# Kernel tuning notes

Hardware: AMD Instinct MI355X
Metric: run time of the kernel (lower is better)

## Reference

```python
import jax, jax.numpy as jnp
import numpy as np

L = 6        # num_coupling_layers
T_DIM = 64   # t_dim
HALF = T_DIM // 2
COND = 128   # cond_dim
HID = 1024   # hidden_dim
B = 32768


def setup_inputs() -> dict:
    key = jax.random.key(0)
    ks = jax.random.split(key, 8)
    s_in = 1.0 / np.sqrt(HALF + COND)
    s_h = 1.0 / np.sqrt(HID)
    T = jax.random.normal(ks[0], (B, T_DIM), dtype=jnp.float32)
    cond = jax.random.normal(ks[1], (B, COND), dtype=jnp.float32)
    W1 = jax.random.normal(ks[2], (L, HALF + COND, HID), dtype=jnp.float32) * s_in
    b1 = jnp.zeros((L, HID), dtype=jnp.float32)
    W2 = jax.random.normal(ks[3], (L, HID, HID), dtype=jnp.float32) * s_h
    b2 = jnp.zeros((L, HID), dtype=jnp.float32)
    W3 = jax.random.normal(ks[4], (L, HID, 2 * HALF), dtype=jnp.float32) * s_h
    b3 = jnp.zeros((L, 2 * HALF), dtype=jnp.float32)
    return {"T": T, "cond": cond, "W1": W1, "b1": b1, "W2": W2, "b2": b2, "W3": W3, "b3": b3}


def reference(T, cond, W1, b1, W2, b2, W3, b3):
    # Conditional normalizing flow: 6 affine coupling layers with alternating
    # contiguous half masks. Even layers transform the first half, odd the second.
    def mlp(h, i):
        x = jax.nn.relu(h @ W1[i] + b1[i])
        x = jax.nn.relu(x @ W2[i] + b2[i])
        return x @ W3[i] + b3[i]

    z = T
    log_det = jnp.zeros(T.shape[0], dtype=T.dtype)
    for i in range(L):
        if i % 2 == 0:
            masked, unmasked = z[:, :HALF], z[:, HALF:]
        else:
            masked, unmasked = z[:, HALF:], z[:, :HALF]
        params = mlp(jnp.concatenate([unmasked, cond], axis=1), i)
        s = jnp.tanh(params[:, :HALF])
        t_shift = params[:, HALF:]
        y_masked = masked * jnp.exp(s) + t_shift
        if i % 2 == 0:
            z = jnp.concatenate([y_masked, unmasked], axis=1)
        else:
            z = jnp.concatenate([unmasked, y_masked], axis=1)
        log_det = log_det + jnp.sum(s, axis=1)
    return z, log_det
```

## Files before the change

### kernel.cpp

```cpp
#include <hip/hip_runtime.h>
#include <hip/hip_fp16.h>
#include <stdint.h>

typedef _Float16 f16;
typedef _Float16 f16x8 __attribute__((ext_vector_type(8)));
typedef float f32x4 __attribute__((ext_vector_type(4)));

#define NB 32768
#define LAYERS 6
#define AK 160
#define HID 1024

__device__ __forceinline__ void async_copy16(const void* g, void* l) {
  __builtin_amdgcn_global_load_lds(
      (const __attribute__((address_space(1))) void*)g,
      (__attribute__((address_space(3))) void*)l, 16, 0, 0);
}

__device__ __forceinline__ void wtrans_tile(const float* __restrict__ W,
                                            f16* __restrict__ Wt,
                                            const int K_, const int N_,
                                            const int bx, const int by,
                                            const int bz, float (*t)[65])
{
  const long off = (long)bz * K_ * N_;
  const float* Wl = W + off;
  f16* Wtl = Wt + off;
  const int k0 = by * 64, n0 = bx * 64;
  const int tx = threadIdx.x & 63, ty4 = threadIdx.x >> 6;
#pragma unroll
  for (int r = ty4; r < 64; r += 4) {
    const int k = k0 + r;
    if (k < K_) t[r][tx] = Wl[(long)k * N_ + n0 + tx];
  }
  __syncthreads();
  const int k = k0 + tx;
  if (k < K_) {
#pragma unroll
    for (int r = ty4; r < 64; r += 4) {
      const int n = n0 + r;
      Wtl[(long)n * K_ + k] = (f16)t[tx][r];
    }
  }
}

__global__ void prep_all(const float* __restrict__ T, const float* __restrict__ cond,
                         const float* __restrict__ W1, const float* __restrict__ W2,
                         const float* __restrict__ W3,
                         float* __restrict__ z, float* __restrict__ ld,
                         f16* __restrict__ A,
                         f16* __restrict__ W1t, f16* __restrict__ W2t,
                         f16* __restrict__ W3t)
{
  __shared__ float t[64][65];
  const int b = blockIdx.x;
  if (b < 2048) {
    const int S1 = NB * 64;
    const int S2 = S1 + NB;
    const int S3 = S2 + NB * 32;
    const int S4 = S3 + NB * 128;
    for (int i = b * blockDim.x + threadIdx.x; i < S4; i += 2048 * blockDim.x) {
      if (i < S1) {
        z[i] = T[i];
      } else if (i < S2) {
        ld[i - S1] = 0.0f;
      } else if (i < S3) {
        int r = i - S2;
        int row = r >> 5, j = r & 31;
        A[(size_t)row * AK + j] = (f16)T[row * 64 + 32 + j];
      } else {
        int r = i - S3;
        int row = r >> 7, j = r & 127;
        A[(size_t)row * AK + 32 + j] = (f16)cond[r];
      }
    }
  } else if (b < 2048 + 288) {
    const int l = b - 2048;
    wtrans_tile(W1, W1t, AK, 1024, l % 16, (l / 16) % 3, l / 48, t);
  } else if (b < 2048 + 288 + 1536) {
    const int l = b - (2048 + 288);
    wtrans_tile(W2, W2t, HID, 1024, l % 16, (l / 16) % 16, l / 256, t);
  } else {
    const int l = b - (2048 + 288 + 1536);
    wtrans_tile(W3, W3t, HID, 64, 0, l % 16, l / 16, t);
  }
}

__global__ __launch_bounds__(256, 2)
void gemm1_full(const f16* __restrict__ A,
                const f16* __restrict__ Wt,
                const float* __restrict__ bias,
                f16* __restrict__ C)
{
  __shared__ __align__(16) f16 As[128 * 160];
  __shared__ __align__(16) f16 Bs[128 * 160];
  const int tid  = threadIdx.x;
  const int lane = tid & 63;
  const int wave = tid >> 6;
  const int c15  = lane & 15;
  const int quad = lane >> 4;
  const int wm = (wave & 1) * 64;
  const int wn = (wave >> 1) * 64;

  const int b = blockIdx.x;
  const int x = b & 7, i = b >> 3;
  const long rowStart = (long)(x * 32 + (i >> 3)) * 128;
  const long colStart = (long)(i & 7) * 128;

  const f16* Ab = A  + rowStart * AK;
  const f16* Bb = Wt + colStart * AK;

#pragma unroll
  for (int it = 0; it < 10; ++it) {
    const int f = it * 256 + tid;
    const int row = f / 20;
    const int ch  = f - row * 20;
    const int chs = ch ^ ((row >> 1) & 3);
    async_copy16(Ab + (long)row * AK + chs * 8, &As[0] + (long)f * 8);
    async_copy16(Bb + (long)row * AK + chs * 8, &Bs[0] + (long)f * 8);
  }
  __syncthreads();

  f32x4 acc[4][4] = {};
#pragma unroll
  for (int kt = 0; kt < 5; ++kt) {
    f16x8 a[4], bf[4];
#pragma unroll
    for (int mi = 0; mi < 4; ++mi) {
      const int R = wm + mi * 16 + c15;
      a[mi] = *(const f16x8*)&As[(R * 20 + kt * 4 + (quad ^ ((R >> 1) & 3))) * 8];
    }
#pragma unroll
    for (int ni = 0; ni < 4; ++ni) {
      const int R = wn + ni * 16 + c15;
      bf[ni] = *(const f16x8*)&Bs[(R * 20 + kt * 4 + (quad ^ ((R >> 1) & 3))) * 8];
    }
#pragma unroll
    for (int mi = 0; mi < 4; ++mi)
#pragma unroll
      for (int ni = 0; ni < 4; ++ni)
        acc[mi][ni] = __builtin_amdgcn_mfma_f32_16x16x32_f16(
            a[mi], bf[ni], acc[mi][ni], 0, 0, 0);
  }

#pragma unroll
  for (int ni = 0; ni < 4; ++ni) {
    const long gn = colStart + wn + ni * 16 + c15;
    const float bv = bias[gn];
#pragma unroll
    for (int mi = 0; mi < 4; ++mi) {
#pragma unroll
      for (int r = 0; r < 4; ++r) {
        const long gm = rowStart + wm + mi * 16 + quad * 4 + r;
        float v = acc[mi][ni][r] + bv;
        v = fmaxf(v, 0.0f);
        C[gm * HID + gn] = (f16)v;
      }
    }
  }
}

__global__ __launch_bounds__(512, 2)
void gemm2_sp(const f16* __restrict__ A,
              const f16* __restrict__ Wt,
              const float* __restrict__ bias,
              f16* __restrict__ C)
{
  __shared__ __align__(16) f16 As[2][8192];
  __shared__ __align__(16) f16 Bs[2][8192];

  const int tid  = threadIdx.x;
  const int lane = tid & 63;
  const int wave = tid >> 6;
  const int c15  = lane & 15;
  const int quad = lane >> 4;
  const int wm = (wave >> 2) * 128;
  const int wn = (wave & 3) * 64;

  const int b = blockIdx.x;
  const int wgid = (b & 7) * 64 + (b >> 3);
  const long rowStart = (long)(wgid >> 2) * 256;
  const long colStart = (long)(wgid & 3) * 256;

  const f16* Ab = A  + rowStart * HID;
  const f16* Bb = Wt + colStart * HID;

  const int r0  = tid >> 2;
  const int ch0 = tid & 3;
  const long g0 = (long)r0 * HID + (((ch0 ^ ((r0 >> 1) & 3))) << 3);
  const int l0 = tid << 3;

  auto stageFull = [&](int kt2, int sel) {
    const f16* sa = Ab + (long)kt2 * 32;
    const f16* sb = Bb + (long)kt2 * 32;
    f16* da = &As[sel][0];
    f16* db = &Bs[sel][0];
    async_copy16(sa + g0,                  da + l0);
    async_copy16(sa + (long)128 * HID + g0, da + 4096 + l0);
    async_copy16(sb + g0,                  db + l0);
    async_copy16(sb + (long)128 * HID + g0, db + 4096 + l0);
  };

  stageFull(0, 0);
  stageFull(1, 1);
  asm volatile("s_waitcnt vmcnt(4)" ::: "memory");
  __builtin_amdgcn_s_barrier();
  __builtin_amdgcn_sched_barrier(0);

  f32x4 acc[8][4] = {};

#pragma unroll 2
  for (int kt = 0; kt < 32; ++kt) {
    const int sel = kt & 1;
    const f16* as = &As[sel][0];
    const f16* bs = &Bs[sel][0];
    const int ktp2 = (kt + 2 < 32) ? kt + 2 : 31;

    f16x8 a[8], bf[4];
#pragma unroll
    for (int m = 0; m < 8; ++m) {
      const int r = wm + m * 16 + c15;
      a[m] = *(const f16x8*)&as[r * 32 + ((quad ^ ((r >> 1) & 3)) << 3)];
    }
#pragma unroll
    for (int n = 0; n < 4; ++n) {
      const int r = wn + n * 16 + c15;
      bf[n] = *(const f16x8*)&bs[r * 32 + ((quad ^ ((r >> 1) & 3)) << 3)];
    }
    asm volatile("s_waitcnt lgkmcnt(0)" ::: "memory");
    __builtin_amdgcn_s_barrier();
    stageFull(ktp2, sel);
    __builtin_amdgcn_sched_barrier(0);
    __builtin_amdgcn_s_setprio(1);
#pragma unroll
    for (int m = 0; m < 8; ++m)
#pragma unroll
      for (int n = 0; n < 4; ++n)
        acc[m][n] = __builtin_amdgcn_mfma_f32_16x16x32_f16(
            a[m], bf[n], acc[m][n], 0, 0, 0);
    __builtin_amdgcn_s_setprio(0);
    __builtin_amdgcn_sched_barrier(0);
    asm volatile("s_waitcnt vmcnt(4)" ::: "memory");
    __builtin_amdgcn_s_barrier();
  }

#pragma unroll
  for (int n = 0; n < 4; ++n) {
    const long gn = colStart + wn + n * 16 + c15;
    const float bv = bias[gn];
#pragma unroll
    for (int m = 0; m < 8; ++m) {
#pragma unroll
      for (int r = 0; r < 4; ++r) {
        const long gm = rowStart + wm + m * 16 + quad * 4 + r;
        float v = acc[m][n][r] + bv;
        C[gm * HID + gn] = (f16)fmaxf(v, 0.0f);
      }
    }
  }
}

__global__ __launch_bounds__(256, 2)
void gemm3_coupling(const f16* __restrict__ X2, const f16* __restrict__ W3t,
                    const float* __restrict__ b3, float* __restrict__ z,
                    float* __restrict__ log_det, f16* __restrict__ Anext,
                    const int maskoff)
{
  __shared__ __align__(16) f16 As[2][64 * 64];
  __shared__ __align__(16) f16 Bs[2][64 * 64];
  const int tid = threadIdx.x;
  const int wave = tid >> 6, lane = tid & 63;
  const int c15 = lane & 15, quad = lane >> 4;
  const int wm = wave * 16;
  const long rowStart = (long)blockIdx.x * 64;

  const f16* Ab = X2 + rowStart * HID;
  const int brow = tid >> 3;
  const int bkc  = ((tid & 7) ^ (brow & 7)) * 8;

  f32x4 acc[4] = {};

  auto stage = [&](int c, int sel) {
    const long kb = (long)c * 64;
#pragma unroll
    for (int q = 0; q < 2; ++q) {
      async_copy16(Ab  + (long)(q * 32 + brow) * HID + kb + bkc,
                   &As[sel][0] + (q * 256 + wave * 64) * 8);
      async_copy16(W3t + (long)(q * 32 + brow) * HID + kb + bkc,
                   &Bs[sel][0] + (q * 256 + wave * 64) * 8);
    }
  };

  stage(0, 0);
  for (int c = 0; c < 16; ++c) {
    __syncthreads();
    if (c + 1 < 16) stage(c + 1, (c + 1) & 1);
    const f16* as = &As[c & 1][0];
    const f16* bs = &Bs[c & 1][0];

#pragma unroll
    for (int s = 0; s < 2; ++s) {
      const int Ra = wm + c15;
      f16x8 a = *(const f16x8*)&as[(Ra * 8 + ((s * 4 + quad) ^ (Ra & 7))) * 8];
      f16x8 bf[4];
#pragma unroll
      for (int ni = 0; ni < 4; ++ni) {
        const int R = ni * 16 + c15;
        bf[ni] = *(const f16x8*)&bs[(R * 8 + ((s * 4 + quad) ^ (R & 7))) * 8];
      }
#pragma unroll
      for (int ni = 0; ni < 4; ++ni)
        acc[ni] = __builtin_amdgcn_mfma_f32_16x16x32_f16(a, bf[ni], acc[ni], 0, 0, 0);
    }
  }

  float sp[4] = {0.0f, 0.0f, 0.0f, 0.0f};
#pragma unroll
  for (int ni = 0; ni < 2; ++ni) {
    const int j = ni * 16 + c15;
    const float bs = b3[j];
    const float bt = b3[32 + j];
#pragma unroll
    for (int r = 0; r < 4; ++r) {
      const long gm = rowStart + wm + quad * 4 + r;
      const float sv = acc[ni][r] + bs;
      const float e2 = __expf(2.0f * sv);
      const float s  = 1.0f - 2.0f / (e2 + 1.0f);
      const float tv = acc[ni + 2][r] + bt;
      const float m  = z[gm * 64 + maskoff + j];
      const float y  = fmaf(m, __expf(s), tv);
      z[gm * 64 + maskoff + j] = y;
      Anext[gm * AK + j] = (f16)y;
      sp[r] += s;
    }
  }
#pragma unroll
  for (int r = 0; r < 4; ++r) {
    float v = sp[r];
    v += __shfl_xor(v, 1);
    v += __shfl_xor(v, 2);
    v += __shfl_xor(v, 4);
    v += __shfl_xor(v, 8);
    if (c15 == 0) {
      const long gm = rowStart + wm + quad * 4 + r;
      log_det[gm] += v;
    }
  }
}

extern "C" void kernel_launch(void* const* d_in, const int* in_sizes, int n_in,
                              void* d_out, int out_size, void* d_ws, size_t ws_size,
                              hipStream_t stream) {
  (void)in_sizes; (void)n_in; (void)out_size; (void)ws_size;
  const float* T    = (const float*)d_in[0];
  const float* cond = (const float*)d_in[1];
  const float* W1   = (const float*)d_in[2];
  const float* b1   = (const float*)d_in[3];
  const float* W2   = (const float*)d_in[4];
  const float* b2   = (const float*)d_in[5];
  const float* W3   = (const float*)d_in[6];
  const float* b3   = (const float*)d_in[7];

  float* z  = (float*)d_out;
  float* ld = z + (size_t)NB * 64;

  f16* A   = (f16*)d_ws;
  f16* X1  = A   + (size_t)NB * AK;
  f16* X2  = X1  + (size_t)NB * HID;
  f16* W1t = X2  + (size_t)NB * HID;
  f16* W2t = W1t + (size_t)6 * 1024 * 160;
  f16* W3t = W2t + ((size_t)6 << 20);

  prep_all<<<3968, 256, 0, stream>>>(T, cond, W1, W2, W3,
                                     z, ld, A, W1t, W2t, W3t);

  const int g1 = (NB / 128) * (HID / 128);
  const int g2 = (NB / 256) * (HID / 256);
  for (int l = 0; l < LAYERS; ++l) {
    gemm1_full<<<g1, 256, 0, stream>>>(A, W1t + (size_t)l * 1024 * AK,
                                       b1 + l * 1024, X1);
    gemm2_sp<<<g2, 512, 0, stream>>>(X1, W2t + ((size_t)l << 20),
                                     b2 + l * 1024, X2);
    const int maskoff = (l & 1) ? 32 : 0;
    gemm3_coupling<<<NB / 64, 256, 0, stream>>>(X2, W3t + (size_t)l * 64 * 1024,
                                                b3 + l * 64, z, ld, A, maskoff);
  }
}
```

Measured before the change: 811.5 us.

## Restructure hidden GEMM into 8-phase ping-pong pipeline with K=64 tiles

```diff
diff --git a/kernel.cpp b/kernel.cpp
--- a/kernel.cpp
+++ b/kernel.cpp
@@ -160,14 +160,44 @@
   }
 }
 
+#define RD_A(dst, base, mq) \
+  _Pragma("unroll") \
+  for (int mi = 0; mi < 4; ++mi) { \
+    const int r_ = wm + (mq) * 64 + mi * 16 + c15; \
+    _Pragma("unroll") \
+    for (int ks = 0; ks < 2; ++ks) \
+      dst[mi][ks] = *(const f16x8*)&(base)[r_ * 64 + ((((ks << 2) + quad) ^ (r_ & 7)) << 3)]; \
+  }
+#define RD_B(dst, base, nq) \
+  _Pragma("unroll") \
+  for (int ni = 0; ni < 2; ++ni) { \
+    const int r_ = wn + (nq) * 32 + ni * 16 + c15; \
+    _Pragma("unroll") \
+    for (int ks = 0; ks < 2; ++ks) \
+      dst[ni][ks] = *(const f16x8*)&(base)[r_ * 64 + ((((ks << 2) + quad) ^ (r_ & 7)) << 3)]; \
+  }
+#define MM(am, an, afr, bfr) \
+  __builtin_amdgcn_s_setprio(1); \
+  _Pragma("unroll") \
+  for (int ks = 0; ks < 2; ++ks) \
+  _Pragma("unroll") \
+  for (int mi = 0; mi < 4; ++mi) \
+  _Pragma("unroll") \
+  for (int ni = 0; ni < 2; ++ni) \
+    acc[(am) + mi][(an) + ni] = __builtin_amdgcn_mfma_f32_16x16x32_f16( \
+        afr[mi][ks], bfr[ni][ks], acc[(am) + mi][(an) + ni], 0, 0, 0); \
+  __builtin_amdgcn_s_setprio(0);
+#define BARRIER __builtin_amdgcn_s_barrier()
+#define LGKM0   asm volatile("s_waitcnt lgkmcnt(0)")
+
 __global__ __launch_bounds__(512, 2)
-void gemm2_sp(const f16* __restrict__ A,
+void gemm2_8p(const f16* __restrict__ A,
               const f16* __restrict__ Wt,
               const float* __restrict__ bias,
               f16* __restrict__ C)
 {
-  __shared__ __align__(16) f16 As[2][8192];
-  __shared__ __align__(16) f16 Bs[2][8192];
+  __shared__ __align__(16) f16 As[2][16384];
+  __shared__ __align__(16) f16 Bs[2][16384];
 
   const int tid  = threadIdx.x;
   const int lane = tid & 63;
@@ -185,75 +215,106 @@
   const f16* Ab = A  + rowStart * HID;
   const f16* Bb = Wt + colStart * HID;
 
-  const int r0  = tid >> 2;
-  const int ch0 = tid & 3;
-  const long g0 = (long)r0 * HID + (((ch0 ^ ((r0 >> 1) & 3))) << 3);
+  const int rh0 = tid >> 3;
+  const int ch0 = tid & 7;
+  const long g0 = (long)rh0 * HID + ((ch0 ^ (rh0 & 7)) << 3);
+  const long g1 = (long)(64 + rh0) * HID + ((ch0 ^ ((64 + rh0) & 7)) << 3);
   const int l0 = tid << 3;
-
-  auto stageFull = [&](int kt2, int sel) {
-    const f16* sa = Ab + (long)kt2 * 32;
-    const f16* sb = Bb + (long)kt2 * 32;
-    f16* da = &As[sel][0];
-    f16* db = &Bs[sel][0];
-    async_copy16(sa + g0,                  da + l0);
-    async_copy16(sa + (long)128 * HID + g0, da + 4096 + l0);
-    async_copy16(sb + g0,                  db + l0);
-    async_copy16(sb + (long)128 * HID + g0, db + 4096 + l0);
+  const int l1 = (512 + tid) << 3;
+
+  auto stA = [&](int kt, int h) {
+    const f16* src = Ab + (long)h * 128 * HID + (long)kt * 64;
+    f16* dst = &As[kt & 1][h * 8192];
+    async_copy16(src + g0, dst + l0);
+    async_copy16(src + g1, dst + l1);
   };
-
-  stageFull(0, 0);
-  stageFull(1, 1);
-  asm volatile("s_waitcnt vmcnt(4)" ::: "memory");
-  __builtin_amdgcn_s_barrier();
-  __builtin_amdgcn_sched_barrier(0);
+  auto stB = [&](int kt, int h) {
+    const f16* src = Bb + (long)h * 128 * HID + (long)kt * 64;
+    f16* dst = &Bs[kt & 1][h * 8192];
+    async_copy16(src + g0, dst + l0);
+    async_copy16(src + g1, dst + l1);
+  };
+
+  stB(0, 0); stA(0, 0); stB(0, 1); stA(0, 1);
+  stB(1, 0); stA(1, 0);
+  asm volatile("s_waitcnt vmcnt(4)");
+  BARRIER;
 
   f32x4 acc[8][4] = {};
 
-#pragma unroll 2
-  for (int kt = 0; kt < 32; ++kt) {
-    const int sel = kt & 1;
-    const f16* as = &As[sel][0];
-    const f16* bs = &Bs[sel][0];
-    const int ktp2 = (kt + 2 < 32) ? kt + 2 : 31;
-
-    f16x8 a[8], bf[4];
-#pragma unroll
-    for (int m = 0; m < 8; ++m) {
-      const int r = wm + m * 16 + c15;
-      a[m] = *(const f16x8*)&as[r * 32 + ((quad ^ ((r >> 1) & 3)) << 3)];
-    }
-#pragma unroll
-    for (int n = 0; n < 4; ++n) {
-      const int r = wn + n * 16 + c15;
-      bf[n] = *(const f16x8*)&bs[r * 32 + ((quad ^ ((r >> 1) & 3)) << 3)];
-    }
-    asm volatile("s_waitcnt lgkmcnt(0)" ::: "memory");
-    __builtin_amdgcn_s_barrier();
-    stageFull(ktp2, sel);
-    __builtin_amdgcn_sched_barrier(0);
-    __builtin_amdgcn_s_setprio(1);
-#pragma unroll
-    for (int m = 0; m < 8; ++m)
-#pragma unroll
-      for (int n = 0; n < 4; ++n)
-        acc[m][n] = __builtin_amdgcn_mfma_f32_16x16x32_f16(
-            a[m], bf[n], acc[m][n], 0, 0, 0);
-    __builtin_amdgcn_s_setprio(0);
-    __builtin_amdgcn_sched_barrier(0);
-    asm volatile("s_waitcnt vmcnt(4)" ::: "memory");
-    __builtin_amdgcn_s_barrier();
-  }
-
-#pragma unroll
-  for (int n = 0; n < 4; ++n) {
-    const long gn = colStart + wn + n * 16 + c15;
+#pragma unroll 1
+  for (int t = 0; t < 8; ++t) {
+    const int kt0 = 2 * t, kt1 = 2 * t + 1;
+    const f16* asx = &As[0][0];
+    const f16* bsx = &Bs[0][0];
+    const f16* asy = &As[1][0];
+    const f16* bsy = &Bs[1][0];
+    const bool pre = (t < 7);
+    f16x8 a0[4][2], a1[4][2], b0[2][2], b1[2][2];
+
+    RD_A(a0, asx, 0);
+    RD_B(b0, bsx, 0);
+    stB(kt1, 1);
+    BARRIER; LGKM0;
+    MM(0, 0, a0, b0);
+    BARRIER;
+
+    RD_B(b1, bsx, 1);
+    stA(kt1, 1);
+    BARRIER; LGKM0;
+    MM(0, 2, a0, b1);
+    BARRIER;
+
+    RD_A(a1, asx, 1);
+    if (pre) stB(kt0 + 2, 0);
+    BARRIER; LGKM0;
+    MM(4, 0, a1, b0);
+    BARRIER;
+
+    if (pre) stA(kt0 + 2, 0);
+    MM(4, 2, a1, b1);
+    if (pre) { asm volatile("s_waitcnt vmcnt(4)"); }
+    else     { asm volatile("s_waitcnt vmcnt(0)"); }
+    BARRIER;
+
+    RD_A(a0, asy, 0);
+    RD_B(b0, bsy, 0);
+    if (pre) stB(kt0 + 2, 1);
+    BARRIER; LGKM0;
+    MM(0, 0, a0, b0);
+    BARRIER;
+
+    RD_B(b1, bsy, 1);
+    if (pre) stA(kt0 + 2, 1);
+    BARRIER; LGKM0;
+    MM(0, 2, a0, b1);
+    BARRIER;
+
+    RD_A(a1, asy, 1);
+    if (pre) stB(kt1 + 2, 0);
+    BARRIER; LGKM0;
+    MM(4, 0, a1, b0);
+    BARRIER;
+
+    if (pre) stA(kt1 + 2, 0);
+    MM(4, 2, a1, b1);
+    if (pre) { asm volatile("s_waitcnt vmcnt(4)"); }
+    else     { asm volatile("s_waitcnt vmcnt(0)"); }
+    BARRIER;
+  }
+
+#pragma unroll
+  for (int nii = 0; nii < 4; ++nii) {
+    const int nof = (nii >> 1) * 32 + (nii & 1) * 16;
+    const long gn = colStart + wn + nof + c15;
     const float bv = bias[gn];
 #pragma unroll
-    for (int m = 0; m < 8; ++m) {
+    for (int mii = 0; mii < 8; ++mii) {
+      const int mof = (mii >> 2) * 64 + (mii & 3) * 16;
 #pragma unroll
       for (int r = 0; r < 4; ++r) {
-        const long gm = rowStart + wm + m * 16 + quad * 4 + r;
-        float v = acc[m][n][r] + bv;
+        const long gm = rowStart + wm + mof + quad * 4 + r;
+        float v = acc[mii][nii][r] + bv;
         C[gm * HID + gn] = (f16)fmaxf(v, 0.0f);
       }
     }
@@ -379,7 +440,7 @@
   for (int l = 0; l < LAYERS; ++l) {
     gemm1_full<<<g1, 256, 0, stream>>>(A, W1t + (size_t)l * 1024 * AK,
                                        b1 + l * 1024, X1);
-    gemm2_sp<<<g2, 512, 0, stream>>>(X1, W2t + ((size_t)l << 20),
+    gemm2_8p<<<g2, 512, 0, stream>>>(X1, W2t + ((size_t)l << 20),
                                      b2 + l * 1024, X2);
     const int maskoff = (l & 1) ? 32 : 0;
     gemm3_coupling<<<NB / 64, 256, 0, stream>>>(X2, W3t + (size_t)l * 64 * 1024,
```

Result: no change. 826.7 us (+1.9%).

## Double K-tile depth in hidden GEMM and stage epilogues through LDS for vector stores

Applied to the files above, without the earlier changes.

```diff
diff --git a/kernel.cpp b/kernel.cpp
--- a/kernel.cpp
+++ b/kernel.cpp
@@ -143,31 +143,42 @@
             a[mi], bf[ni], acc[mi][ni], 0, 0, 0);
   }
 
+  __syncthreads();
+  f16* Lp = &As[0] + wave * 4096;
+  const int erow = lane >> 3;
+  const int ec   = lane & 7;
 #pragma unroll
   for (int ni = 0; ni < 4; ++ni) {
     const long gn = colStart + wn + ni * 16 + c15;
     const float bv = bias[gn];
+    const int lc = ni * 16 + c15;
 #pragma unroll
     for (int mi = 0; mi < 4; ++mi) {
 #pragma unroll
       for (int r = 0; r < 4; ++r) {
-        const long gm = rowStart + wm + mi * 16 + quad * 4 + r;
+        const int R = mi * 16 + quad * 4 + r;
         float v = acc[mi][ni][r] + bv;
-        v = fmaxf(v, 0.0f);
-        C[gm * HID + gn] = (f16)v;
+        Lp[R * 64 + (((lc >> 3) ^ (quad << 1)) << 3) + (lc & 7)] = (f16)fmaxf(v, 0.0f);
       }
     }
   }
+#pragma unroll
+  for (int it = 0; it < 8; ++it) {
+    const int R = it * 8 + erow;
+    const int phys = ec ^ (((R >> 2) & 3) << 1);
+    f16x8 rowv = *(const f16x8*)&Lp[R * 64 + (phys << 3)];
+    *(f16x8*)&C[(rowStart + wm + R) * HID + colStart + wn + ec * 8] = rowv;
+  }
 }
 
 __global__ __launch_bounds__(512, 2)
-void gemm2_sp(const f16* __restrict__ A,
-              const f16* __restrict__ Wt,
-              const float* __restrict__ bias,
-              f16* __restrict__ C)
+void gemm2_v1b(const f16* __restrict__ A,
+               const f16* __restrict__ Wt,
+               const float* __restrict__ bias,
+               f16* __restrict__ C)
 {
-  __shared__ __align__(16) f16 As[2][8192];
-  __shared__ __align__(16) f16 Bs[2][8192];
+  __shared__ __align__(16) f16 As[2][16384];
+  __shared__ __align__(16) f16 Bs[2][16384];
 
   const int tid  = threadIdx.x;
   const int lane = tid & 63;
@@ -185,78 +196,104 @@
   const f16* Ab = A  + rowStart * HID;
   const f16* Bb = Wt + colStart * HID;
 
-  const int r0  = tid >> 2;
-  const int ch0 = tid & 3;
-  const long g0 = (long)r0 * HID + (((ch0 ^ ((r0 >> 1) & 3))) << 3);
+  const int rh0 = tid >> 3;
+  const int ch0 = tid & 7;
+  const long g0 = (long)rh0 * HID + ((ch0 ^ (rh0 & 7)) << 3);
+  const long g1 = (long)(64 + rh0) * HID + ((ch0 ^ ((64 + rh0) & 7)) << 3);
   const int l0 = tid << 3;
+  const int l1 = (512 + tid) << 3;
 
   auto stageFull = [&](int kt2, int sel) {
-    const f16* sa = Ab + (long)kt2 * 32;
-    const f16* sb = Bb + (long)kt2 * 32;
+    const f16* sa = Ab + (long)kt2 * 64;
+    const f16* sb = Bb + (long)kt2 * 64;
     f16* da = &As[sel][0];
     f16* db = &Bs[sel][0];
-    async_copy16(sa + g0,                  da + l0);
-    async_copy16(sa + (long)128 * HID + g0, da + 4096 + l0);
-    async_copy16(sb + g0,                  db + l0);
-    async_copy16(sb + (long)128 * HID + g0, db + 4096 + l0);
+    async_copy16(sa + g0, da + l0);
+    async_copy16(sa + (long)128 * HID + g0, da + 8192 + l0);
+    async_copy16(sa + g1, da + l1);
+    async_copy16(sa + (long)128 * HID + g1, da + 8192 + l1);
+    async_copy16(sb + g0, db + l0);
+    async_copy16(sb + (long)128 * HID + g0, db + 8192 + l0);
+    async_copy16(sb + g1, db + l1);
+    async_copy16(sb + (long)128 * HID + g1, db + 8192 + l1);
   };
 
   stageFull(0, 0);
   stageFull(1, 1);
-  asm volatile("s_waitcnt vmcnt(4)" ::: "memory");
+  asm volatile("s_waitcnt vmcnt(8)" ::: "memory");
   __builtin_amdgcn_s_barrier();
-  __builtin_amdgcn_sched_barrier(0);
 
   f32x4 acc[8][4] = {};
 
 #pragma unroll 2
-  for (int kt = 0; kt < 32; ++kt) {
+  for (int kt = 0; kt < 16; ++kt) {
     const int sel = kt & 1;
     const f16* as = &As[sel][0];
     const f16* bs = &Bs[sel][0];
-    const int ktp2 = (kt + 2 < 32) ? kt + 2 : 31;
-
-    f16x8 a[8], bf[4];
+
+    f16x8 a[8][2], bf[4][2];
 #pragma unroll
     for (int m = 0; m < 8; ++m) {
       const int r = wm + m * 16 + c15;
-      a[m] = *(const f16x8*)&as[r * 32 + ((quad ^ ((r >> 1) & 3)) << 3)];
+#pragma unroll
+      for (int ks = 0; ks < 2; ++ks)
+        a[m][ks] = *(const f16x8*)&as[r * 64 + ((((ks << 2) + quad) ^ (r & 7)) << 3)];
     }
 #pragma unroll
     for (int n = 0; n < 4; ++n) {
       const int r = wn + n * 16 + c15;
-      bf[n] = *(const f16x8*)&bs[r * 32 + ((quad ^ ((r >> 1) & 3)) << 3)];
+#pragma unroll
+      for (int ks = 0; ks < 2; ++ks)
+        bf[n][ks] = *(const f16x8*)&bs[r * 64 + ((((ks << 2) + quad) ^ (r & 7)) << 3)];
     }
     asm volatile("s_waitcnt lgkmcnt(0)" ::: "memory");
     __builtin_amdgcn_s_barrier();
-    stageFull(ktp2, sel);
-    __builtin_amdgcn_sched_barrier(0);
+    if (kt + 2 < 16) stageFull(kt + 2, sel);
     __builtin_amdgcn_s_setprio(1);
 #pragma unroll
-    for (int m = 0; m < 8; ++m)
-#pragma unroll
-      for (int n = 0; n < 4; ++n)
-        acc[m][n] = __builtin_amdgcn_mfma_f32_16x16x32_f16(
-            a[m], bf[n], acc[m][n], 0, 0, 0);
+    for (int ks = 0; ks < 2; ++ks)
+#pragma unroll
+      for (int m = 0; m < 8; ++m)
+#pragma unroll
+        for (int n = 0; n < 4; ++n)
+          acc[m][n] = __builtin_amdgcn_mfma_f32_16x16x32_f16(
+              a[m][ks], bf[n][ks], acc[m][n], 0, 0, 0);
     __builtin_amdgcn_s_setprio(0);
-    __builtin_amdgcn_sched_barrier(0);
-    asm volatile("s_waitcnt vmcnt(4)" ::: "memory");
+    if (kt + 2 < 16) {
+      asm volatile("s_waitcnt vmcnt(8)" ::: "memory");
+    } else if (kt + 1 < 16) {
+      asm volatile("s_waitcnt vmcnt(0)" ::: "memory");
+    }
     __builtin_amdgcn_s_barrier();
   }
 
-#pragma unroll
-  for (int n = 0; n < 4; ++n) {
-    const long gn = colStart + wn + n * 16 + c15;
-    const float bv = bias[gn];
-#pragma unroll
-    for (int m = 0; m < 8; ++m) {
+  f16* Lp = &As[0][0] + wave * 1024;
+  const int erow = lane >> 3;
+  const int ec   = lane & 7;
+  const int ecol8 = ec * 8;
+  const long gcol = colStart + wn;
+  const int q0x = ((erow >> 2) & 3) << 1;
+  const int q1x = (((8 + erow) >> 2) & 3) << 1;
+#pragma unroll
+  for (int mii = 0; mii < 8; ++mii) {
+    const int mof = (mii >> 2) * 64 + (mii & 3) * 16;
+#pragma unroll
+    for (int nii = 0; nii < 4; ++nii) {
+      const int nof = (nii >> 1) * 32 + (nii & 1) * 16;
+      const float bv = bias[gcol + nof + c15];
+      const int lc = nof + c15;
 #pragma unroll
       for (int r = 0; r < 4; ++r) {
-        const long gm = rowStart + wm + m * 16 + quad * 4 + r;
-        float v = acc[m][n][r] + bv;
-        C[gm * HID + gn] = (f16)fmaxf(v, 0.0f);
+        float v = acc[mii][nii][r] + bv;
+        Lp[(quad * 4 + r) * 64 + (((lc >> 3) ^ (quad << 1)) << 3) + (lc & 7)]
+            = (f16)fmaxf(v, 0.0f);
       }
     }
+    f16x8 row0 = *(const f16x8*)&Lp[erow * 64 + ((ec ^ q0x) << 3)];
+    f16x8 row1 = *(const f16x8*)&Lp[(8 + erow) * 64 + ((ec ^ q1x) << 3)];
+    const long gm0 = rowStart + wm + mof + erow;
+    *(f16x8*)&C[gm0 * HID + gcol + ecol8] = row0;
+    *(f16x8*)&C[(gm0 + 8) * HID + gcol + ecol8] = row1;
   }
 }
 
@@ -379,8 +416,8 @@
   for (int l = 0; l < LAYERS; ++l) {
     gemm1_full<<<g1, 256, 0, stream>>>(A, W1t + (size_t)l * 1024 * AK,
                                        b1 + l * 1024, X1);
-    gemm2_sp<<<g2, 512, 0, stream>>>(X1, W2t + ((size_t)l << 20),
-                                     b2 + l * 1024, X2);
+    gemm2_v1b<<<g2, 512, 0, stream>>>(X1, W2t + ((size_t)l << 20),
+                                      b2 + l * 1024, X2);
     const int maskoff = (l & 1) ? 32 : 0;
     gemm3_coupling<<<NB / 64, 256, 0, stream>>>(X2, W3t + (size_t)l * 64 * 1024,
                                                 b3 + l * 64, z, ld, A, maskoff);
```

Result: slower. 911.5 us (+12.3%).
